# Kernel optimization log

Hardware: AMD Instinct MI355X
Metric: run time of the kernel (lower is better)

The kernel has to match this reference:

```python
import jax, jax.numpy as jnp
import numpy as np


def _base_index(H, W, dtype=jnp.float32):
    # Homogeneous pixel coordinates (x, y, 1) per pixel, shape [H, W, 3].
    x = jnp.arange(W, dtype=dtype)
    y = jnp.arange(H, dtype=dtype)
    xx, yy = jnp.meshgrid(x, y)  # [H, W]
    return jnp.stack([xx, yy, jnp.ones_like(xx)], axis=-1)


def _bilinear_resample(image, coords):
    # image: [B, H, W, C]; coords: [B, H, W, 2] in (x, y) order (tf resampler convention).
    # Out-of-bounds corners contribute zero (zero padding), matching tfa.image.resampler.
    B, H, W, C = image.shape
    x = coords[..., 0]
    y = coords[..., 1]
    x0 = jnp.floor(x)
    y0 = jnp.floor(y)
    wx1 = x - x0
    wy1 = y - y0
    wx0 = 1.0 - wx1
    wy0 = 1.0 - wy1
    x0i = x0.astype(jnp.int32)
    y0i = y0.astype(jnp.int32)
    x1i = x0i + 1
    y1i = y0i + 1

    def corner(yi, xi, w):
        valid = (xi >= 0) & (xi < W) & (yi >= 0) & (yi < H)
        xc = jnp.clip(xi, 0, W - 1)
        yc = jnp.clip(yi, 0, H - 1)
        # gather per batch: [B, H, W, C]
        g = jax.vmap(lambda im, yy, xx: im[yy, xx])(image, yc, xc)
        return g * (w * valid.astype(image.dtype))[..., None]

    return (corner(y0i, x0i, wy0 * wx0) + corner(y0i, x1i, wy0 * wx1)
            + corner(y1i, x0i, wy1 * wx0) + corner(y1i, x1i, wy1 * wx1))


def setup_inputs() -> dict:
    key = jax.random.key(0)
    k1, k2, k3 = jax.random.split(key, 3)
    B, H, W, C = 4, 512, 640, 16
    image_tensor = jax.random.normal(k1, (B, H, W, C), dtype=jnp.float32)
    # positive depths around 1
    depth_tensor = 0.5 + jax.random.uniform(k2, (B, H, W), dtype=jnp.float32)
    # near-identity projective transform so sampled coords land mostly in-bounds
    eye = jnp.eye(4, dtype=jnp.float32)[None].repeat(B, axis=0)
    project_tensor = eye + 0.001 * jax.random.normal(k3, (B, 4, 4), dtype=jnp.float32)
    return {"image_tensor": image_tensor, "depth_tensor": depth_tensor,
            "project_tensor": project_tensor}


def reference(image_tensor, depth_tensor, project_tensor):
    B, H, W, C = image_tensor.shape
    base = _base_index(H, W, image_tensor.dtype)  # [H, W, 3]
    R = project_tensor[:, :3, :3]                 # [B, 3, 3]
    t = project_tensor[:, :3, 3]                  # [B, 3]
    # tf.tensordot(R, base, [-1,-1]) -> [B,3,H,W]; transpose -> [B,H,W,3]
    rotate = jnp.einsum('bij,hwj->bhwi', R, base)
    sample = rotate * depth_tensor[..., None] + t[:, None, None, :]  # [B,H,W,3]
    coords = sample[..., :2] / sample[..., 2:3]                       # [B,H,W,2] (x,y)
    return _bilinear_resample(image_tensor, coords)
```

## Files before the change

kernel.cpp:

```cpp
#include <hip/hip_runtime.h>

constexpr int B  = 4;
constexpr int H  = 512;
constexpr int Wd = 640;
constexpr int C  = 16;
constexpr int NPIX = B * H * Wd;
constexpr int NTHREADS = NPIX * (C / 4);

__global__ __launch_bounds__(256) void depth_project_kernel(
    const float* __restrict__ image,
    const float* __restrict__ depth,
    const float* __restrict__ proj,
    float4* __restrict__ out)
{
    int tid = blockIdx.x * blockDim.x + threadIdx.x;
    if (tid >= NTHREADS) return;

    int c4  = tid & 3;
    int pix = tid >> 2;
    int w   = pix % Wd;
    int t   = pix / Wd;
    int h   = t % H;
    int b   = t / H;

    const float* P = proj + b * 16;
    float x = (float)w;
    float y = (float)h;
    float d = depth[pix];

    float sx = (P[0] * x + P[1] * y + P[2])  * d + P[3];
    float sy = (P[4] * x + P[5] * y + P[6])  * d + P[7];
    float sz = (P[8] * x + P[9] * y + P[10]) * d + P[11];
    float cx = sx / sz;
    float cy = sy / sz;

    float x0f = floorf(cx), y0f = floorf(cy);
    float wx1 = cx - x0f,   wy1 = cy - y0f;
    float wx0 = 1.0f - wx1, wy0 = 1.0f - wy1;
    int x0 = (int)x0f, y0 = (int)y0f;
    int x1 = x0 + 1,   y1 = y0 + 1;

    float vx0 = (x0 >= 0 && x0 < Wd) ? 1.0f : 0.0f;
    float vx1 = (x1 >= 0 && x1 < Wd) ? 1.0f : 0.0f;
    float vy0 = (y0 >= 0 && y0 < H)  ? 1.0f : 0.0f;
    float vy1 = (y1 >= 0 && y1 < H)  ? 1.0f : 0.0f;

    int x0c = min(max(x0, 0), Wd - 1);
    int x1c = min(max(x1, 0), Wd - 1);
    int y0c = min(max(y0, 0), H - 1);
    int y1c = min(max(y1, 0), H - 1);

    float w00 = wy0 * wx0 * vy0 * vx0;
    float w01 = wy0 * wx1 * vy0 * vx1;
    float w10 = wy1 * wx0 * vy1 * vx0;
    float w11 = wy1 * wx1 * vy1 * vx1;

    const float4* img4 = (const float4*)image;
    int base_b = b * (H * Wd * 4);
    float4 g00 = img4[base_b + (y0c * Wd + x0c) * 4 + c4];
    float4 g01 = img4[base_b + (y0c * Wd + x1c) * 4 + c4];
    float4 g10 = img4[base_b + (y1c * Wd + x0c) * 4 + c4];
    float4 g11 = img4[base_b + (y1c * Wd + x1c) * 4 + c4];

    float4 r;
    r.x = g00.x * w00 + g01.x * w01 + g10.x * w10 + g11.x * w11;
    r.y = g00.y * w00 + g01.y * w01 + g10.y * w10 + g11.y * w11;
    r.z = g00.z * w00 + g01.z * w01 + g10.z * w10 + g11.z * w11;
    r.w = g00.w * w00 + g01.w * w01 + g10.w * w10 + g11.w * w11;

    out[tid] = r;
}

extern "C" void kernel_launch(void* const* d_in, const int* in_sizes, int n_in,
                              void* d_out, int out_size, void* d_ws, size_t ws_size,
                              hipStream_t stream) {
    const float* image = (const float*)d_in[0];
    const float* depth = (const float*)d_in[1];
    const float* proj  = (const float*)d_in[2];
    float4* out = (float4*)d_out;

    constexpr int block = 256;
    constexpr int grid  = (NTHREADS + block - 1) / block;
    depth_project_kernel<<<grid, block, 0, stream>>>(image, depth, proj, out);
}
```

Before: 157.2 us.

## Stage image tile halo in LDS and sample bilinear corners from shared memory

Restructures the kernel so each block handles a 16x32 pixel output tile and first loads a 21x39 halo region of the image (all 16 channels) into shared memory. Bilinear corner reads come from LDS when all four corners fall inside the halo, with a fallback to global gathers otherwise. Each thread now processes two full pixels (16 channels each) rather than one float4 channel group. It also uses a fast reciprocal in place of division and nontemporal stores for the output. The intent is to cut redundant global gather traffic, at the cost of an extra tile load, a barrier and a less coalesced per-thread store pattern.

```diff
diff --git a/kernel.cpp b/kernel.cpp
--- a/kernel.cpp
+++ b/kernel.cpp
@@ -3,72 +3,118 @@
 constexpr int B  = 4;
 constexpr int H  = 512;
 constexpr int Wd = 640;
-constexpr int C  = 16;
-constexpr int NPIX = B * H * Wd;
-constexpr int NTHREADS = NPIX * (C / 4);
+
+constexpr int TR = 16, TC = 32;
+constexpr int RR = 21, RC = 39;
+constexpr int TILES_X = Wd / TC;
+constexpr int TILES_Y = H  / TR;
+constexpr int CHUNKS  = RR * RC * 4;
+
+typedef float f32x4 __attribute__((ext_vector_type(4)));
 
 __global__ __launch_bounds__(256) void depth_project_kernel(
     const float* __restrict__ image,
     const float* __restrict__ depth,
     const float* __restrict__ proj,
-    float4* __restrict__ out)
+    f32x4* __restrict__ out)
 {
-    int tid = blockIdx.x * blockDim.x + threadIdx.x;
-    if (tid >= NTHREADS) return;
+    __shared__ f32x4 s_img[RR * RC * 4];
 
-    int c4  = tid & 3;
-    int pix = tid >> 2;
-    int w   = pix % Wd;
-    int t   = pix / Wd;
-    int h   = t % H;
-    int b   = t / H;
+    int blk = blockIdx.x;
+    int txt = blk % TILES_X;
+    int tyt = (blk / TILES_X) % TILES_Y;
+    int b   = blk / (TILES_X * TILES_Y);
+    int x0t = txt * TC;
+    int y0t = tyt * TR;
+    int ry0 = min(max(y0t - 3, 0), H - RR);
+    int rx0 = min(max(x0t - 3, 0), Wd - RC);
 
+    const f32x4* __restrict__ img4 = (const f32x4*)image;
+    int imgbase = b * (H * Wd * 4);
     const float* P = proj + b * 16;
-    float x = (float)w;
-    float y = (float)h;
-    float d = depth[pix];
+    float P0 = P[0], P1 = P[1], P2  = P[2],  P3  = P[3];
+    float P4 = P[4], P5 = P[5], P6  = P[6],  P7  = P[7];
+    float P8 = P[8], P9 = P[9], P10 = P[10], P11 = P[11];
 
-    float sx = (P[0] * x + P[1] * y + P[2])  * d + P[3];
-    float sy = (P[4] * x + P[5] * y + P[6])  * d + P[7];
-    float sz = (P[8] * x + P[9] * y + P[10]) * d + P[11];
-    float cx = sx / sz;
-    float cy = sy / sz;
+    int tid = threadIdx.x;
 
-    float x0f = floorf(cx), y0f = floorf(cy);
-    float wx1 = cx - x0f,   wy1 = cy - y0f;
-    float wx0 = 1.0f - wx1, wy0 = 1.0f - wy1;
-    int x0 = (int)x0f, y0 = (int)y0f;
-    int x1 = x0 + 1,   y1 = y0 + 1;
+    for (int i = tid; i < CHUNKS; i += 256) {
+        int r   = i / (RC * 4);
+        int rem = i - r * (RC * 4);
+        int gx  = rx0 + (rem >> 2);
+        int c4  = rem & 3;
+        int pix = (ry0 + r) * Wd + gx;
+        s_img[i] = img4[imgbase + pix * 4 + c4];
+    }
+    __syncthreads();
 
-    float vx0 = (x0 >= 0 && x0 < Wd) ? 1.0f : 0.0f;
-    float vx1 = (x1 >= 0 && x1 < Wd) ? 1.0f : 0.0f;
-    float vy0 = (y0 >= 0 && y0 < H)  ? 1.0f : 0.0f;
-    float vy1 = (y1 >= 0 && y1 < H)  ? 1.0f : 0.0f;
+    #pragma unroll
+    for (int pp = 0; pp < 2; pp++) {
+        int lp = tid + pp * 256;
+        int px = lp & (TC - 1);
+        int py = lp >> 5;
+        int gx = x0t + px;
+        int gy = y0t + py;
+        int gpix = gy * Wd + gx;
 
-    int x0c = min(max(x0, 0), Wd - 1);
-    int x1c = min(max(x1, 0), Wd - 1);
-    int y0c = min(max(y0, 0), H - 1);
-    int y1c = min(max(y1, 0), H - 1);
+        float d = depth[b * H * Wd + gpix];
+        float x = (float)gx, y = (float)gy;
+        float sx = (P0 * x + P1 * y + P2)  * d + P3;
+        float sy = (P4 * x + P5 * y + P6)  * d + P7;
+        float sz = (P8 * x + P9 * y + P10) * d + P11;
+        float rz = __builtin_amdgcn_rcpf(sz);
+        float cx = sx * rz;
+        float cy = sy * rz;
 
-    float w00 = wy0 * wx0 * vy0 * vx0;
-    float w01 = wy0 * wx1 * vy0 * vx1;
-    float w10 = wy1 * wx0 * vy1 * vx0;
-    float w11 = wy1 * wx1 * vy1 * vx1;
+        float x0f = floorf(cx), y0f = floorf(cy);
+        float wx1 = cx - x0f,   wy1 = cy - y0f;
+        float wx0 = 1.0f - wx1, wy0 = 1.0f - wy1;
+        int x0 = (int)x0f, y0 = (int)y0f;
+        int x1 = x0 + 1,   y1 = y0 + 1;
 
-    const float4* img4 = (const float4*)image;
-    int base_b = b * (H * Wd * 4);
-    float4 g00 = img4[base_b + (y0c * Wd + x0c) * 4 + c4];
-    float4 g01 = img4[base_b + (y0c * Wd + x1c) * 4 + c4];
-    float4 g10 = img4[base_b + (y1c * Wd + x0c) * 4 + c4];
-    float4 g11 = img4[base_b + (y1c * Wd + x1c) * 4 + c4];
+        float vx0 = (x0 >= 0 && x0 < Wd) ? 1.0f : 0.0f;
+        float vx1 = (x1 >= 0 && x1 < Wd) ? 1.0f : 0.0f;
+        float vy0 = (y0 >= 0 && y0 < H)  ? 1.0f : 0.0f;
+        float vy1 = (y1 >= 0 && y1 < H)  ? 1.0f : 0.0f;
 
-    float4 r;
-    r.x = g00.x * w00 + g01.x * w01 + g10.x * w10 + g11.x * w11;
-    r.y = g00.y * w00 + g01.y * w01 + g10.y * w10 + g11.y * w11;
-    r.z = g00.z * w00 + g01.z * w01 + g10.z * w10 + g11.z * w11;
-    r.w = g00.w * w00 + g01.w * w01 + g10.w * w10 + g11.w * w11;
+        int x0c = min(max(x0, 0), Wd - 1);
+        int x1c = min(max(x1, 0), Wd - 1);
+        int y0c = min(max(y0, 0), H - 1);
+        int y1c = min(max(y1, 0), H - 1);
 
-    out[tid] = r;
+        float w00 = wy0 * wx0 * vy0 * vx0;
+        float w01 = wy0 * wx1 * vy0 * vx1;
+        float w10 = wy1 * wx0 * vy1 * vx0;
+        float w11 = wy1 * wx1 * vy1 * vx1;
+
+        f32x4 acc[4];
+        bool inr = (y0c >= ry0) & (y1c <= ry0 + RR - 1) &
+                   (x0c >= rx0) & (x1c <= rx0 + RC - 1);
+        if (inr) {
+            int c00 = ((y0c - ry0) * RC + (x0c - rx0)) * 4;
+            int c01 = ((y0c - ry0) * RC + (x1c - rx0)) * 4;
+            int c10 = ((y1c - ry0) * RC + (x0c - rx0)) * 4;
+            int c11 = ((y1c - ry0) * RC + (x1c - rx0)) * 4;
+            #pragma unroll
+            for (int c = 0; c < 4; c++)
+                acc[c] = s_img[c00 + c] * w00 + s_img[c01 + c] * w01 +
+                         s_img[c10 + c] * w10 + s_img[c11 + c] * w11;
+        } else {
+            int g00 = imgbase + (y0c * Wd + x0c) * 4;
+            int g01 = imgbase + (y0c * Wd + x1c) * 4;
+            int g10 = imgbase + (y1c * Wd + x0c) * 4;
+            int g11 = imgbase + (y1c * Wd + x1c) * 4;
+            #pragma unroll
+            for (int c = 0; c < 4; c++)
+                acc[c] = img4[g00 + c] * w00 + img4[g01 + c] * w01 +
+                         img4[g10 + c] * w10 + img4[g11 + c] * w11;
+        }
+
+        int obase = (b * H * Wd + gpix) * 4;
+        #pragma unroll
+        for (int c = 0; c < 4; c++)
+            __builtin_nontemporal_store(acc[c], out + obase + c);
+    }
 }
 
 extern "C" void kernel_launch(void* const* d_in, const int* in_sizes, int n_in,
@@ -77,9 +123,8 @@
     const float* image = (const float*)d_in[0];
     const float* depth = (const float*)d_in[1];
     const float* proj  = (const float*)d_in[2];
-    float4* out = (float4*)d_out;
+    f32x4* out = (f32x4*)d_out;
 
-    constexpr int block = 256;
-    constexpr int grid  = (NTHREADS + block - 1) / block;
-    depth_project_kernel<<<grid, block, 0, stream>>>(image, depth, proj, out);
+    constexpr int grid = B * TILES_X * TILES_Y;
+    depth_project_kernel<<<grid, 256, 0, stream>>>(image, depth, proj, out);
 }
```

New measurement: 200.0 us. +27.2%, slower.
